# Optimization experiments

Measured on AMD Instinct MI355X. Metric: run time of the kernel, lower is better.

Reference implementation:

```python
import jax, jax.numpy as jnp
import numpy as np

T = 100.0  # temperature, from init_kwargs
B = 4096
D = 128
NUM_CLASSES = 10


def setup_inputs() -> dict:
    key = jax.random.key(0)
    kx, ky = jax.random.split(key)
    x = jax.random.normal(kx, (B, D), dtype=jnp.float32)
    y = jax.random.randint(ky, (B,), 0, NUM_CLASSES, dtype=jnp.int64)
    return {"x": x, "y": y}


def reference(x, y):
    # Pairwise squared Euclidean distances: dist[i,j] = ||x_i - x_j||^2
    sq = jnp.sum(x * x, axis=1)                      # [b]
    dist = sq[:, None] + sq[None, :] - 2.0 * (x @ x.T)  # [b, b]
    dist = jnp.maximum(dist, 0.0)                    # clamp fp error; diag -> 0

    e = jnp.exp(-dist / T)                           # [b, b]; e[i,i] = 1

    b = x.shape[0]
    same = (y[:, None] == y[None, :])                # same-label mask
    not_self = ~jnp.eye(b, dtype=bool)

    # numerator: sum over j != i with y[j] == y[i]
    num = jnp.sum(jnp.where(same & not_self, e, 0.0), axis=1)  # [b]
    # denominator: sum over ALL j, including j == i (exp(0) = 1), as in the
    # original loop where the denominator accumulates unconditionally
    den = jnp.sum(e, axis=1)                         # [b]

    return jnp.mean(-jnp.log(num / den))
```

## Files before the change

kernel.cpp:

```cpp
#include <hip/hip_runtime.h>
#include <hip/hip_bf16.h>

#define NB 4096
#define NT2 64
#define NOFF 2016
#define NTILE 2080

typedef short v8s __attribute__((ext_vector_type(8)));
typedef float v4f __attribute__((ext_vector_type(4)));


__global__ __launch_bounds__(256) void prep_kernel(const float* __restrict__ x,
        float* __restrict__ sq, float* __restrict__ out,
        unsigned short* __restrict__ xb) {
    int tid = threadIdx.x;
    int row = blockIdx.x * 8 + (tid >> 5);
    int lane = tid & 31;
    const float4* xg = (const float4*)x;
    float4 v = xg[row * 32 + lane];
    __hip_bfloat16 h0 = __float2bfloat16(v.x), h1 = __float2bfloat16(v.y);
    __hip_bfloat16 h2 = __float2bfloat16(v.z), h3 = __float2bfloat16(v.w);
    ushort4 u4;
    u4.x = *(unsigned short*)&h0; u4.y = *(unsigned short*)&h1;
    u4.z = *(unsigned short*)&h2; u4.w = *(unsigned short*)&h3;
    ((ushort4*)xb)[row * 32 + lane] = u4;
    float s = v.x * v.x + v.y * v.y + v.z * v.z + v.w * v.w;
    #pragma unroll
    for (int off = 16; off > 0; off >>= 1) s += __shfl_down(s, off);
    if (lane == 0) sq[row] = s;
    if (blockIdx.x == 0 && tid == 0) out[0] = 0.f;
}

__global__ __launch_bounds__(256, 4) void snn64(
        const unsigned short* __restrict__ xb, const int* __restrict__ y,
        const float* __restrict__ sqg, float2* __restrict__ Q2) {
    __shared__ __align__(16) union {
        unsigned short tiles[2 * 64 * 136];
        float2 part[2][64][17];
    } sm;
    __shared__ float2 part2[2][64];
    __shared__ float sqi[64], sqj[64];
    __shared__ int yi[64], yj[64];

    const int tid = threadIdx.x;
    const int wave = tid >> 6;
    const int lane = tid & 63;
    const int wm = wave >> 1, wn = wave & 1;
    const int lr = lane & 15, q = lane >> 4;

    int k = blockIdx.x, bi, bj;
    if (k >= NOFF) { bi = k - NOFF; bj = bi; }
    else {
        int tt = k, rem = 63; bi = 0;
        while (tt >= rem) { tt -= rem; ++bi; --rem; }
        bj = bi + 1 + tt;
    }
    const int i0 = bi * 64, j0 = bj * 64;
    const bool diag = (bi == bj);
    unsigned short* At = sm.tiles;
    unsigned short* Bt = diag ? At : At + 64 * 136;

    const v8s* xg = (const v8s*)xb;
    #pragma unroll
    for (int r = 0; r < 4; ++r) {
        int c = r * 256 + tid;
        int row = c >> 4, cc = c & 15;
        *(v8s*)&At[row * 136 + cc * 8] = xg[(i0 + row) * 16 + cc];
        if (!diag)
            *(v8s*)&Bt[row * 136 + cc * 8] = xg[(j0 + row) * 16 + cc];
    }
    if (tid < 64) {
        sqi[tid] = sqg[i0 + tid]; yi[tid] = y[i0 + tid];
        sqj[tid] = sqg[j0 + tid]; yj[tid] = y[j0 + tid];
    }
    __syncthreads();

    v4f acc[2][2];
    #pragma unroll
    for (int mt = 0; mt < 2; ++mt)
        #pragma unroll
        for (int nt = 0; nt < 2; ++nt)
            acc[mt][nt] = (v4f){0.f, 0.f, 0.f, 0.f};
    #pragma unroll
    for (int kk = 0; kk < 4; ++kk) {
        v8s a0 = *(const v8s*)&At[(wm * 32 + lr) * 136 + kk * 32 + q * 8];
        v8s a1 = *(const v8s*)&At[(wm * 32 + 16 + lr) * 136 + kk * 32 + q * 8];
        v8s b0 = *(const v8s*)&Bt[(wn * 32 + lr) * 136 + kk * 32 + q * 8];
        v8s b1 = *(const v8s*)&Bt[(wn * 32 + 16 + lr) * 136 + kk * 32 + q * 8];
        acc[0][0] = __builtin_amdgcn_mfma_f32_16x16x32_bf16(a0, b0, acc[0][0], 0, 0, 0);
        acc[0][1] = __builtin_amdgcn_mfma_f32_16x16x32_bf16(a0, b1, acc[0][1], 0, 0, 0);
        acc[1][0] = __builtin_amdgcn_mfma_f32_16x16x32_bf16(a1, b0, acc[1][0], 0, 0, 0);
        acc[1][1] = __builtin_amdgcn_mfma_f32_16x16x32_bf16(a1, b1, acc[1][1], 0, 0, 0);
    }
    __syncthreads();

    float sqj_r[2]; int yj_r[2], jgl[2];
    #pragma unroll
    for (int nt = 0; nt < 2; ++nt) {
        int jc = wn * 32 + nt * 16 + lr;
        sqj_r[nt] = sqj[jc]; yj_r[nt] = yj[jc]; jgl[nt] = j0 + jc;
    }
    float cn[2] = {0.f, 0.f}, cd[2] = {0.f, 0.f};
    #pragma unroll
    for (int mt = 0; mt < 2; ++mt)
        #pragma unroll
        for (int r = 0; r < 4; ++r) {
            int rloc = wm * 32 + mt * 16 + q * 4 + r;
            float si = sqi[rloc]; int yir = yi[rloc]; int ig = i0 + rloc;
            float n = 0.f, d = 0.f;
            #pragma unroll
            for (int nt = 0; nt < 2; ++nt) {
                float dist = fmaxf(si + sqj_r[nt] - 2.f * acc[mt][nt][r], 0.f);
                float e = __builtin_amdgcn_exp2f(dist * -0.014426950408889634f);
                float me = (yir == yj_r[nt] && ig != jgl[nt]) ? e : 0.f;
                d += e; n += me;
                cd[nt] += e; cn[nt] += me;
            }
            sm.part[wn][rloc][lr] = make_float2(n, d);
        }
    #pragma unroll
    for (int nt = 0; nt < 2; ++nt) {
        float n2 = cn[nt] + __shfl_xor(cn[nt], 16); n2 += __shfl_xor(n2, 32);
        float d2 = cd[nt] + __shfl_xor(cd[nt], 16); d2 += __shfl_xor(d2, 32);
        if (q == 0) part2[wm][wn * 32 + nt * 16 + lr] = make_float2(n2, d2);
    }
    __syncthreads();

    if (tid < 128) {
        int row = tid >> 1, h = tid & 1;
        float sn = 0.f, sd = 0.f;
        #pragma unroll
        for (int c = 0; c < 16; ++c) {
            float2 v = sm.part[h][row][c]; sn += v.x; sd += v.y;
        }
        sn += __shfl_down(sn, 1); sd += __shfl_down(sd, 1);
        if (h == 0) Q2[bj * NB + i0 + row] = make_float2(sn, sd);
    }
    if (!diag && tid < 64) {
        float2 a = part2[0][tid], b = part2[1][tid];
        Q2[bi * NB + j0 + tid] = make_float2(a.x + b.x, a.y + b.y);
    }
}

__global__ __launch_bounds__(256) void snn_final(const float2* __restrict__ Q2,
        float* __restrict__ out) {
    __shared__ float wsum[4];
    int i = blockIdx.x * 256 + threadIdx.x;
    float n = 0.f, d = 0.f;
    #pragma unroll 8
    for (int b = 0; b < NT2; ++b) {
        float2 v = Q2[b * NB + i];
        n += v.x; d += v.y;
    }
    float l = -__logf(n / d);
    #pragma unroll
    for (int off = 32; off > 0; off >>= 1) l += __shfl_down(l, off);
    if ((threadIdx.x & 63) == 0) wsum[threadIdx.x >> 6] = l;
    __syncthreads();
    if (threadIdx.x == 0)
        atomicAdd(out, (wsum[0] + wsum[1] + wsum[2] + wsum[3]) * (1.0f / NB));
}

extern "C" void kernel_launch(void* const* d_in, const int* in_sizes, int n_in,
                              void* d_out, int out_size, void* d_ws, size_t ws_size,
                              hipStream_t stream) {
    const float* x = (const float*)d_in[0];
    const int*   y = (const int*)d_in[1];
    float* out = (float*)d_out;
    float* sq  = (float*)d_ws;
    unsigned short* xb = (unsigned short*)(sq + NB);
    float2* Q2 = (float2*)(xb + NB * 128);

    prep_kernel<<<NB / 8, 256, 0, stream>>>(x, sq, out, xb);
    snn64<<<NTILE, 256, 0, stream>>>(xb, y, sq, Q2);
    snn_final<<<NB / 256, 256, 0, stream>>>(Q2, out);
}
```

Baseline: 73.84 us.

## Make tile kernel persistent with double-buffered LDS prefetch of next tile

Replaces the one-tile-per-block launch with 512 persistent blocks that each process 4-5 tiles strided by the grid size. The global-to-LDS load of the next tile is issued before the current tile's MFMA and epilogue, so load latency can overlap compute. The partial-sum scratch now reuses the current tile buffer instead of a union. The cost is double the LDS per block and lower occupancy (launch bounds 2), plus extra syncs per iteration. Because stage writes LDS directly through registers, much of the load latency may still sit in front of the compute.

Measured after the change: 79.01 us. 1.07x slower.

```diff
diff --git a/kernel.cpp b/kernel.cpp
--- a/kernel.cpp
+++ b/kernel.cpp
@@ -5,6 +5,7 @@
 #define NT2 64
 #define NOFF 2016
 #define NTILE 2080
+#define PBLK 512
 
 typedef short v8s __attribute__((ext_vector_type(8)));
 typedef float v4f __attribute__((ext_vector_type(4)));
@@ -31,114 +32,134 @@
     if (blockIdx.x == 0 && tid == 0) out[0] = 0.f;
 }
 
-__global__ __launch_bounds__(256, 4) void snn64(
+__global__ __launch_bounds__(256, 2) void snn64p(
         const unsigned short* __restrict__ xb, const int* __restrict__ y,
         const float* __restrict__ sqg, float2* __restrict__ Q2) {
-    __shared__ __align__(16) union {
-        unsigned short tiles[2 * 64 * 136];
-        float2 part[2][64][17];
-    } sm;
+    __shared__ __align__(16) unsigned short tiles[2][2 * 64 * 136];
     __shared__ float2 part2[2][64];
-    __shared__ float sqi[64], sqj[64];
-    __shared__ int yi[64], yj[64];
+    __shared__ float sqi[2][64], sqj[2][64];
+    __shared__ int yi[2][64], yj[2][64];
 
     const int tid = threadIdx.x;
     const int wave = tid >> 6;
     const int lane = tid & 63;
     const int wm = wave >> 1, wn = wave & 1;
     const int lr = lane & 15, q = lane >> 4;
+    const v8s* xg = (const v8s*)xb;
 
-    int k = blockIdx.x, bi, bj;
-    if (k >= NOFF) { bi = k - NOFF; bj = bi; }
-    else {
-        int tt = k, rem = 63; bi = 0;
-        while (tt >= rem) { tt -= rem; ++bi; --rem; }
-        bj = bi + 1 + tt;
-    }
-    const int i0 = bi * 64, j0 = bj * 64;
-    const bool diag = (bi == bj);
-    unsigned short* At = sm.tiles;
-    unsigned short* Bt = diag ? At : At + 64 * 136;
+    const int bid = blockIdx.x;
+    const int ntiles = (bid < NTILE - 4 * PBLK) ? 5 : 4;
 
-    const v8s* xg = (const v8s*)xb;
-    #pragma unroll
-    for (int r = 0; r < 4; ++r) {
-        int c = r * 256 + tid;
-        int row = c >> 4, cc = c & 15;
-        *(v8s*)&At[row * 136 + cc * 8] = xg[(i0 + row) * 16 + cc];
-        if (!diag)
-            *(v8s*)&Bt[row * 136 + cc * 8] = xg[(j0 + row) * 16 + cc];
-    }
-    if (tid < 64) {
-        sqi[tid] = sqg[i0 + tid]; yi[tid] = y[i0 + tid];
-        sqj[tid] = sqg[j0 + tid]; yj[tid] = y[j0 + tid];
-    }
+    auto decode = [](int k, int& bi, int& bj) {
+        if (k >= NOFF) { bi = k - NOFF; bj = bi; }
+        else {
+            int tt = k, rem = 63; bi = 0;
+            while (tt >= rem) { tt -= rem; ++bi; --rem; }
+            bj = bi + 1 + tt;
+        }
+    };
+
+    auto stage = [&](int k, int buf) {
+        int bi, bj; decode(k, bi, bj);
+        int i0 = bi * 64, j0 = bj * 64;
+        bool dg = (bi == bj);
+        unsigned short* At = tiles[buf];
+        unsigned short* Bt = At + 64 * 136;
+        #pragma unroll
+        for (int r = 0; r < 4; ++r) {
+            int c = r * 256 + tid;
+            int row = c >> 4, cc = c & 15;
+            *(v8s*)&At[row * 136 + cc * 8] = xg[(i0 + row) * 16 + cc];
+            if (!dg)
+                *(v8s*)&Bt[row * 136 + cc * 8] = xg[(j0 + row) * 16 + cc];
+        }
+        if (tid < 64) {
+            sqi[buf][tid] = sqg[i0 + tid]; yi[buf][tid] = y[i0 + tid];
+            sqj[buf][tid] = sqg[j0 + tid]; yj[buf][tid] = y[j0 + tid];
+        }
+    };
+
+    stage(bid, 0);
     __syncthreads();
 
-    v4f acc[2][2];
-    #pragma unroll
-    for (int mt = 0; mt < 2; ++mt)
+    for (int s = 0; s < ntiles; ++s) {
+        const int buf = s & 1;
+        const int k = bid + s * PBLK;
+        int bi, bj; decode(k, bi, bj);
+        const int i0 = bi * 64, j0 = bj * 64;
+        const bool diag = (bi == bj);
+
+        if (s + 1 < ntiles) stage(bid + (s + 1) * PBLK, buf ^ 1);
+
+        unsigned short* At = tiles[buf];
+        unsigned short* Bt = diag ? At : At + 64 * 136;
+
+        v4f acc[2][2];
         #pragma unroll
-        for (int nt = 0; nt < 2; ++nt)
-            acc[mt][nt] = (v4f){0.f, 0.f, 0.f, 0.f};
-    #pragma unroll
-    for (int kk = 0; kk < 4; ++kk) {
-        v8s a0 = *(const v8s*)&At[(wm * 32 + lr) * 136 + kk * 32 + q * 8];
-        v8s a1 = *(const v8s*)&At[(wm * 32 + 16 + lr) * 136 + kk * 32 + q * 8];
-        v8s b0 = *(const v8s*)&Bt[(wn * 32 + lr) * 136 + kk * 32 + q * 8];
-        v8s b1 = *(const v8s*)&Bt[(wn * 32 + 16 + lr) * 136 + kk * 32 + q * 8];
-        acc[0][0] = __builtin_amdgcn_mfma_f32_16x16x32_bf16(a0, b0, acc[0][0], 0, 0, 0);
-        acc[0][1] = __builtin_amdgcn_mfma_f32_16x16x32_bf16(a0, b1, acc[0][1], 0, 0, 0);
-        acc[1][0] = __builtin_amdgcn_mfma_f32_16x16x32_bf16(a1, b0, acc[1][0], 0, 0, 0);
-        acc[1][1] = __builtin_amdgcn_mfma_f32_16x16x32_bf16(a1, b1, acc[1][1], 0, 0, 0);
-    }
-    __syncthreads();
+        for (int mt = 0; mt < 2; ++mt)
+            #pragma unroll
+            for (int nt = 0; nt < 2; ++nt)
+                acc[mt][nt] = (v4f){0.f, 0.f, 0.f, 0.f};
+        #pragma unroll
+        for (int kk = 0; kk < 4; ++kk) {
+            v8s a0 = *(const v8s*)&At[(wm * 32 + lr) * 136 + kk * 32 + q * 8];
+            v8s a1 = *(const v8s*)&At[(wm * 32 + 16 + lr) * 136 + kk * 32 + q * 8];
+            v8s b0 = *(const v8s*)&Bt[(wn * 32 + lr) * 136 + kk * 32 + q * 8];
+            v8s b1 = *(const v8s*)&Bt[(wn * 32 + 16 + lr) * 136 + kk * 32 + q * 8];
+            acc[0][0] = __builtin_amdgcn_mfma_f32_16x16x32_bf16(a0, b0, acc[0][0], 0, 0, 0);
+            acc[0][1] = __builtin_amdgcn_mfma_f32_16x16x32_bf16(a0, b1, acc[0][1], 0, 0, 0);
+            acc[1][0] = __builtin_amdgcn_mfma_f32_16x16x32_bf16(a1, b0, acc[1][0], 0, 0, 0);
+            acc[1][1] = __builtin_amdgcn_mfma_f32_16x16x32_bf16(a1, b1, acc[1][1], 0, 0, 0);
+        }
 
-    float sqj_r[2]; int yj_r[2], jgl[2];
-    #pragma unroll
-    for (int nt = 0; nt < 2; ++nt) {
-        int jc = wn * 32 + nt * 16 + lr;
-        sqj_r[nt] = sqj[jc]; yj_r[nt] = yj[jc]; jgl[nt] = j0 + jc;
-    }
-    float cn[2] = {0.f, 0.f}, cd[2] = {0.f, 0.f};
-    #pragma unroll
-    for (int mt = 0; mt < 2; ++mt)
+        float2* partp = (float2*)At;
+        float sqj_r[2]; int yj_r[2], jgl[2];
         #pragma unroll
-        for (int r = 0; r < 4; ++r) {
-            int rloc = wm * 32 + mt * 16 + q * 4 + r;
-            float si = sqi[rloc]; int yir = yi[rloc]; int ig = i0 + rloc;
-            float n = 0.f, d = 0.f;
+        for (int nt = 0; nt < 2; ++nt) {
+            int jc = wn * 32 + nt * 16 + lr;
+            sqj_r[nt] = sqj[buf][jc]; yj_r[nt] = yj[buf][jc]; jgl[nt] = j0 + jc;
+        }
+        float cn[2] = {0.f, 0.f}, cd[2] = {0.f, 0.f};
+        #pragma unroll
+        for (int mt = 0; mt < 2; ++mt)
             #pragma unroll
-            for (int nt = 0; nt < 2; ++nt) {
-                float dist = fmaxf(si + sqj_r[nt] - 2.f * acc[mt][nt][r], 0.f);
-                float e = __builtin_amdgcn_exp2f(dist * -0.014426950408889634f);
-                float me = (yir == yj_r[nt] && ig != jgl[nt]) ? e : 0.f;
-                d += e; n += me;
-                cd[nt] += e; cn[nt] += me;
+            for (int r = 0; r < 4; ++r) {
+                int rloc = wm * 32 + mt * 16 + q * 4 + r;
+                float si = sqi[buf][rloc]; int yir = yi[buf][rloc]; int ig = i0 + rloc;
+                float n = 0.f, d = 0.f;
+                #pragma unroll
+                for (int nt = 0; nt < 2; ++nt) {
+                    float dist = fmaxf(si + sqj_r[nt] - 2.f * acc[mt][nt][r], 0.f);
+                    float e = __builtin_amdgcn_exp2f(dist * -0.014426950408889634f);
+                    float me = (yir == yj_r[nt] && ig != jgl[nt]) ? e : 0.f;
+                    d += e; n += me;
+                    cd[nt] += e; cn[nt] += me;
+                }
+                partp[(wn * 64 + rloc) * 17 + lr] = make_float2(n, d);
             }
-            sm.part[wn][rloc][lr] = make_float2(n, d);
+        #pragma unroll
+        for (int nt = 0; nt < 2; ++nt) {
+            float n2 = cn[nt] + __shfl_xor(cn[nt], 16); n2 += __shfl_xor(n2, 32);
+            float d2 = cd[nt] + __shfl_xor(cd[nt], 16); d2 += __shfl_xor(d2, 32);
+            if (q == 0) part2[wm][wn * 32 + nt * 16 + lr] = make_float2(n2, d2);
         }
-    #pragma unroll
-    for (int nt = 0; nt < 2; ++nt) {
-        float n2 = cn[nt] + __shfl_xor(cn[nt], 16); n2 += __shfl_xor(n2, 32);
-        float d2 = cd[nt] + __shfl_xor(cd[nt], 16); d2 += __shfl_xor(d2, 32);
-        if (q == 0) part2[wm][wn * 32 + nt * 16 + lr] = make_float2(n2, d2);
-    }
-    __syncthreads();
+        __syncthreads();
 
-    if (tid < 128) {
-        int row = tid >> 1, h = tid & 1;
-        float sn = 0.f, sd = 0.f;
-        #pragma unroll
-        for (int c = 0; c < 16; ++c) {
-            float2 v = sm.part[h][row][c]; sn += v.x; sd += v.y;
+        if (tid < 128) {
+            int row = tid >> 1, h = tid & 1;
+            float sn = 0.f, sd = 0.f;
+            #pragma unroll
+            for (int c = 0; c < 16; ++c) {
+                float2 v = partp[(h * 64 + row) * 17 + c]; sn += v.x; sd += v.y;
+            }
+            sn += __shfl_down(sn, 1); sd += __shfl_down(sd, 1);
+            if (h == 0) Q2[bj * NB + i0 + row] = make_float2(sn, sd);
         }
-        sn += __shfl_down(sn, 1); sd += __shfl_down(sd, 1);
-        if (h == 0) Q2[bj * NB + i0 + row] = make_float2(sn, sd);
-    }
-    if (!diag && tid < 64) {
-        float2 a = part2[0][tid], b = part2[1][tid];
-        Q2[bi * NB + j0 + tid] = make_float2(a.x + b.x, a.y + b.y);
+        if (!diag && tid < 64) {
+            float2 a = part2[0][tid], b = part2[1][tid];
+            Q2[bi * NB + j0 + tid] = make_float2(a.x + b.x, a.y + b.y);
+        }
+        __syncthreads();
     }
 }
 
@@ -172,6 +193,6 @@
     float2* Q2 = (float2*)(xb + NB * 128);
 
     prep_kernel<<<NB / 8, 256, 0, stream>>>(x, sq, out, xb);
-    snn64<<<NTILE, 256, 0, stream>>>(xb, y, sq, Q2);
+    snn64p<<<PBLK, 256, 0, stream>>>(xb, y, sq, Q2);
     snn_final<<<NB / 256, 256, 0, stream>>>(Q2, out);
 }
```
